# Kernel tuning notes

Measured on AMD Instinct MI355X. Metric: run time of the kernel, lower is better.

Reference implementation:

```python
import jax, jax.numpy as jnp
import numpy as np

B, S = 1, 1863
D_MODEL, H = 1024, 16
HD = D_MODEL // H  # 64
MAX_X, MAX_Y, MAX_Z = 32, 32, 8
BASE = 10000.0
MAX_DXY, MAX_DZ = 30, 8
N_PAIRS = HD // 2
PX = N_PAIRS // 3  # 10
PY = N_PAIRS // 3  # 10
PZ = N_PAIRS - PX - PY  # 12


def _rotate_half(x):
    # (x0,x1,x2,x3,...) -> (-x1,x0,-x3,x2,...)
    x1 = x[..., ::2]
    x2 = x[..., 1::2]
    return jnp.stack((-x2, x1), axis=-1).reshape(x.shape)


def _rope_tables(max_pos, dim):
    inv = 1.0 / (BASE ** (np.arange(0, dim, 2, dtype=np.float32) / dim))
    f = np.outer(np.arange(max_pos, dtype=np.float32), inv)
    return jnp.asarray(np.cos(f)), jnp.asarray(np.sin(f))


def setup_inputs() -> dict:
    key = jax.random.key(0)
    ks = jax.random.split(key, 8)
    x = jax.random.normal(ks[0], (B, S, D_MODEL), dtype=jnp.float32)
    Wqkv = jax.random.normal(ks[1], (3 * D_MODEL, D_MODEL), dtype=jnp.float32) * 0.02
    Wout = jax.random.normal(ks[2], (D_MODEL, D_MODEL), dtype=jnp.float32) * 0.02
    bias_x = jax.random.normal(ks[3], (2 * MAX_DXY + 1, H), dtype=jnp.float32) * 0.02
    bias_y = jax.random.normal(ks[4], (2 * MAX_DXY + 1, H), dtype=jnp.float32) * 0.02
    bias_z = jax.random.normal(ks[5], (2 * MAX_DZ + 1, H), dtype=jnp.float32) * 0.02
    pos_xyz = jax.random.randint(ks[6], (B, S, 3), 0, 32, dtype=jnp.int32)
    return {"x": x, "Wqkv": Wqkv, "Wout": Wout, "bias_x": bias_x,
            "bias_y": bias_y, "bias_z": bias_z, "pos_xyz": pos_xyz}


def _apply_rope3d(q, k, pos_xyz):
    cx, sx = _rope_tables(MAX_X, 2 * PX)
    cy, sy = _rope_tables(MAX_Y, 2 * PY)
    cz, sz = _rope_tables(MAX_Z, 2 * PZ)
    xp = jnp.clip(pos_xyz[..., 0], 0, MAX_X - 1)
    yp = jnp.clip(pos_xyz[..., 1], 0, MAX_Y - 1)
    zp = jnp.clip(pos_xyz[..., 2], 0, MAX_Z - 1)
    # [B,S,head_dim] after repeat-interleave(2) per axis, then concat
    cos = jnp.concatenate([jnp.repeat(cx[xp], 2, axis=-1),
                           jnp.repeat(cy[yp], 2, axis=-1),
                           jnp.repeat(cz[zp], 2, axis=-1)], axis=-1)[:, :, None, :]
    sin = jnp.concatenate([jnp.repeat(sx[xp], 2, axis=-1),
                           jnp.repeat(sy[yp], 2, axis=-1),
                           jnp.repeat(sz[zp], 2, axis=-1)], axis=-1)[:, :, None, :]
    q_rot = q * cos + _rotate_half(q) * sin
    k_rot = k * cos + _rotate_half(k) * sin
    return q_rot, k_rot


def reference(x, Wqkv, Wout, bias_x, bias_y, bias_z, pos_xyz):
    b, s, _ = x.shape
    qkv = x @ Wqkv.T  # [B,S,3*D]
    q, k, v = jnp.split(qkv, 3, axis=-1)
    q = q.reshape(b, s, H, HD)
    k = k.reshape(b, s, H, HD)
    v = v.reshape(b, s, H, HD)
    q, k = _apply_rope3d(q, k, pos_xyz)
    scores = jnp.einsum('bqhd,bkhd->bhqk', q, k) * (HD ** -0.5)
    # 3D relative position bias
    px_, py_, pz_ = pos_xyz[..., 0], pos_xyz[..., 1], pos_xyz[..., 2]
    dx = jnp.clip(px_[:, :, None] - px_[:, None, :], -MAX_DXY, MAX_DXY) + MAX_DXY
    dy = jnp.clip(py_[:, :, None] - py_[:, None, :], -MAX_DXY, MAX_DXY) + MAX_DXY
    dz = jnp.clip(pz_[:, :, None] - pz_[:, None, :], -MAX_DZ, MAX_DZ) + MAX_DZ
    bias = (bias_x[dx] + bias_y[dy] + bias_z[dz]).transpose(0, 3, 1, 2)  # [B,H,S,S]
    scores = scores + bias
    causal = jnp.tril(jnp.ones((s, s), dtype=bool))
    scores = jnp.where(causal, scores, -jnp.inf)
    attn = jax.nn.softmax(scores, axis=-1)
    out = jnp.einsum('bhqk,bkhd->bqhd', attn, v).reshape(b, s, D_MODEL)
    return out @ Wout.T
```

## Files before the change

kernel.cpp:

```cpp
#include <hip/hip_runtime.h>

typedef __bf16 bf16;
typedef __bf16 bf16x2 __attribute__((ext_vector_type(2)));
typedef __bf16 bf16x4 __attribute__((ext_vector_type(4)));
typedef __bf16 bf16x8 __attribute__((ext_vector_type(8)));
typedef float  f32x4  __attribute__((ext_vector_type(4)));

#define S_LEN 1863
#define S_PAD 1920
#define DM 1024
#define NH 16
#define HDIM 64
#define AUGD 160
#define KA_STR 168
#define QKV_STRIDE 3072
#define NQT128 15
#define CHUNK 4
#define MAXC 8
#define NQMULTI 13
#define NCHUNK_HEAD 64

#define MFMA_BF16 __builtin_amdgcn_mfma_f32_16x16x32_bf16

__constant__ int QT_BASE[15] = {0, 1, 2, 4, 6, 9, 12, 16, 20, 25, 30, 36, 42, 49, 56};

__device__ __forceinline__ void dma16(const bf16* g, bf16* l) {
  __builtin_amdgcn_global_load_lds(
      (const __attribute__((address_space(1))) unsigned int*)g,
      (__attribute__((address_space(3))) unsigned int*)l, 16, 0, 0);
}

__global__ void cvt3(const float* __restrict__ a, bf16* __restrict__ oa, int na4,
                     const float* __restrict__ b, bf16* __restrict__ ob, int nb4,
                     const float* __restrict__ c, bf16* __restrict__ oc, int nc4) {
  int j = blockIdx.x * blockDim.x + threadIdx.x;
  const float* s; bf16* d;
  if (j < na4) { s = a; d = oa; }
  else {
    j -= na4;
    if (j < nb4) { s = b; d = ob; }
    else { j -= nb4; if (j >= nc4) return; s = c; d = oc; }
  }
  float4 v = ((const float4*)s)[j];
  bf16x4 o;
  o[0] = (bf16)v.x; o[1] = (bf16)v.y; o[2] = (bf16)v.z; o[3] = (bf16)v.w;
  ((bf16x4*)d)[j] = o;
}

template <typename T>
__global__ __launch_bounds__(256) void gemm_bt(const bf16* __restrict__ A,
                                               const bf16* __restrict__ B,
                                               T* __restrict__ C,
                                               int M, int N, int K) {
  __shared__ bf16 As[128][40];
  __shared__ bf16 Bs[64][40];
  const int t = threadIdx.x;
  const int w = t >> 6, l = t & 63;
  const int quad = l >> 4, l16 = l & 15;
  const int wm = w >> 1, wn = w & 1;
  const int bm = blockIdx.y * 128, bn = blockIdx.x * 64;

  f32x4 acc[4][2];
#pragma unroll
  for (int mi = 0; mi < 4; ++mi)
#pragma unroll
    for (int ni = 0; ni < 2; ++ni) acc[mi][ni] = 0;

  const int srow = t >> 2;
  const int sk8  = (t & 3) * 8;

  for (int k0 = 0; k0 < K; k0 += 32) {
    bf16x8 a0 = *(const bf16x8*)&A[(size_t)min(bm + srow,      M - 1) * K + k0 + sk8];
    bf16x8 a1 = *(const bf16x8*)&A[(size_t)min(bm + srow + 64, M - 1) * K + k0 + sk8];
    bf16x8 b0 = *(const bf16x8*)&B[(size_t)(bn + srow) * K + k0 + sk8];
    __syncthreads();
    *(bf16x8*)&As[srow][sk8]      = a0;
    *(bf16x8*)&As[srow + 64][sk8] = a1;
    *(bf16x8*)&Bs[srow][sk8]      = b0;
    __syncthreads();

    bf16x8 af[4], bfr[2];
#pragma unroll
    for (int mi = 0; mi < 4; ++mi) af[mi]  = *(bf16x8*)&As[wm * 64 + mi * 16 + l16][quad * 8];
#pragma unroll
    for (int ni = 0; ni < 2; ++ni) bfr[ni] = *(bf16x8*)&Bs[wn * 32 + ni * 16 + l16][quad * 8];
#pragma unroll
    for (int mi = 0; mi < 4; ++mi)
#pragma unroll
      for (int ni = 0; ni < 2; ++ni)
        acc[mi][ni] = MFMA_BF16(af[mi], bfr[ni], acc[mi][ni], 0, 0, 0);
  }

#pragma unroll
  for (int mi = 0; mi < 4; ++mi)
#pragma unroll
    for (int r = 0; r < 4; ++r) {
      int m = bm + wm * 64 + mi * 16 + quad * 4 + r;
      if (m < M) {
#pragma unroll
        for (int ni = 0; ni < 2; ++ni)
          C[(size_t)m * N + bn + wn * 32 + ni * 16 + l16] = (T)acc[mi][ni][r];
      }
    }
}

__global__ __launch_bounds__(256) void gemm_bt64(const bf16* __restrict__ A,
                                                 const bf16* __restrict__ B,
                                                 float* __restrict__ C,
                                                 int M, int N, int K) {
  __shared__ bf16 As[64][40];
  __shared__ bf16 Bs[64][40];
  const int t = threadIdx.x;
  const int w = t >> 6, l = t & 63;
  const int quad = l >> 4, l16 = l & 15;
  const int wm = w >> 1, wn = w & 1;
  const int bm = blockIdx.y * 64, bn = blockIdx.x * 64;

  f32x4 acc[2][2];
#pragma unroll
  for (int mi = 0; mi < 2; ++mi)
#pragma unroll
    for (int ni = 0; ni < 2; ++ni) acc[mi][ni] = 0;

  const int srow = t >> 2;
  const int sk8  = (t & 3) * 8;

  for (int k0 = 0; k0 < K; k0 += 32) {
    bf16x8 a0 = *(const bf16x8*)&A[(size_t)min(bm + srow, M - 1) * K + k0 + sk8];
    bf16x8 b0 = *(const bf16x8*)&B[(size_t)(bn + srow) * K + k0 + sk8];
    __syncthreads();
    *(bf16x8*)&As[srow][sk8] = a0;
    *(bf16x8*)&Bs[srow][sk8] = b0;
    __syncthreads();

    bf16x8 af[2], bfr[2];
#pragma unroll
    for (int mi = 0; mi < 2; ++mi) af[mi]  = *(bf16x8*)&As[wm * 32 + mi * 16 + l16][quad * 8];
#pragma unroll
    for (int ni = 0; ni < 2; ++ni) bfr[ni] = *(bf16x8*)&Bs[wn * 32 + ni * 16 + l16][quad * 8];
#pragma unroll
    for (int mi = 0; mi < 2; ++mi)
#pragma unroll
      for (int ni = 0; ni < 2; ++ni)
        acc[mi][ni] = MFMA_BF16(af[mi], bfr[ni], acc[mi][ni], 0, 0, 0);
  }

#pragma unroll
  for (int mi = 0; mi < 2; ++mi)
#pragma unroll
    for (int r = 0; r < 4; ++r) {
      int m = bm + wm * 32 + mi * 16 + quad * 4 + r;
      if (m < M) {
#pragma unroll
        for (int ni = 0; ni < 2; ++ni)
          C[(size_t)m * N + bn + wn * 32 + ni * 16 + l16] = acc[mi][ni][r];
      }
    }
}

__global__ __launch_bounds__(256) void pack_all(const bf16* __restrict__ qkv,
                                                const int* __restrict__ pos,
                                                const float* __restrict__ bxg,
                                                const float* __restrict__ byg,
                                                const float* __restrict__ bzg,
                                                bf16* __restrict__ Qa,
                                                bf16* __restrict__ Ka,
                                                bf16* __restrict__ Vt) {
  const int st = blockIdx.x, h = blockIdx.y;
  const int t = threadIdx.x;
  __shared__ float bxs[61], bys[61], bzs[17];
  __shared__ float vtile[64][68];

  if (t < 61) { bxs[t] = bxg[t * NH + h]; bys[t] = byg[t * NH + h]; }
  if (t < 17) bzs[t] = bzg[t * NH + h];

  for (int i = t; i < 1024; i += 256) {
    int row = i >> 4, c4 = (i & 15) * 4;
    int sg = min(st * 64 + row, S_LEN - 1);
    bf16x4 v = *(const bf16x4*)&qkv[(size_t)sg * QKV_STRIDE + 2 * DM + h * HDIM + c4];
    *(float4*)&vtile[row][c4] = make_float4((float)v[0], (float)v[1], (float)v[2], (float)v[3]);
  }
  __syncthreads();

  for (int i = t; i < 2048; i += 256) {
    const int sl = i >> 5, sub = i & 31;
    const int s = st * 64 + sl;
    const int sc = min(s, S_LEN - 1);
    const int px = pos[sc * 3 + 0], py = pos[sc * 3 + 1], pz = pos[sc * 3 + 2];
    int j, P, pp;
    if (sub < 10)      { j = sub;      P = 10; pp = min(max(px, 0), 31); }
    else if (sub < 20) { j = sub - 10; P = 10; pp = min(max(py, 0), 31); }
    else               { j = sub - 20; P = 12; pp = min(max(pz, 0), 7);  }
    const float inv = __expf(-(float)j / (float)P * 9.210340371976184f);
    const float ang = (float)pp * inv;
    float sn, cs;
    __sincosf(ang, &sn, &cs);
    const size_t base = (size_t)sc * QKV_STRIDE + h * HDIM + 2 * sub;
    bf16x2 q2 = *(const bf16x2*)&qkv[base];
    bf16x2 k2 = *(const bf16x2*)&qkv[base + DM];
    float q0 = (float)q2[0], q1 = (float)q2[1];
    float k0 = (float)k2[0], k1 = (float)k2[1];
    const size_t qb = ((size_t)h * S_PAD + s) * AUGD;
    const size_t kb = ((size_t)h * S_PAD + s) * KA_STR;
    bf16x2 oq, ok;
    oq[0] = (bf16)((q0 * cs - q1 * sn) * 0.125f);
    oq[1] = (bf16)((q1 * cs + q0 * sn) * 0.125f);
    ok[0] = (bf16)(k0 * cs - k1 * sn);
    ok[1] = (bf16)(k1 * cs + k0 * sn);
    *(bf16x2*)&Qa[qb + 2 * sub] = oq;
    *(bf16x2*)&Ka[kb + 2 * sub] = ok;

    const int ix = min(max(px - sub, -30), 30) + 30;
    const int iy = min(max(py - sub, -30), 30) + 30;
    const int iz = min(max(pz - sub, -8), 8) + 8;
    Qa[qb + 64 + sub]  = (bf16)bxs[ix];
    Qa[qb + 96 + sub]  = (bf16)bys[iy];
    Qa[qb + 128 + sub] = (bf16)bzs[iz];
    Ka[kb + 64 + sub]  = (bf16)(sub == px ? 1.0f : 0.0f);
    Ka[kb + 96 + sub]  = (bf16)(sub == py ? 1.0f : 0.0f);
    Ka[kb + 128 + sub] = (bf16)(sub == pz ? 1.0f : 0.0f);
  }

  for (int i = t; i < 1024; i += 256) {
    int d = i >> 4, s4 = (i & 15) * 4;
    bf16x4 o;
    o[0] = (bf16)vtile[s4 + 0][d];
    o[1] = (bf16)vtile[s4 + 1][d];
    o[2] = (bf16)vtile[s4 + 2][d];
    o[3] = (bf16)vtile[s4 + 3][d];
    *(bf16x4*)&Vt[((size_t)h * HDIM + d) * S_PAD + st * 64 + s4] = o;
  }
}

__global__ __launch_bounds__(256) void attn_split(const bf16* __restrict__ Qa,
                                                  const bf16* __restrict__ Ka,
                                                  const bf16* __restrict__ Vt,
                                                  bf16* __restrict__ outb,
                                                  float* __restrict__ Opart,
                                                  float* __restrict__ lpart) {
  const int b = blockIdx.x;
  const int h = b & 15;
  const int id = 63 - (b >> 4);
  int qt = 14;
  while (QT_BASE[qt] > id) --qt;
  const int c = id - QT_BASE[qt];
  const int chain = 2 * qt + 2;
  const int k0 = c * CHUNK;
  const int kend = min(k0 + CHUNK, chain);

  const int t = threadIdx.x, w = t >> 6, l = t & 63;
  const int quad = l >> 4, l16 = l & 15;

  __shared__ bf16 Ks[64][KA_STR];
  __shared__ bf16 Vs[64][72];
  __shared__ bf16 Ps[4][16][72];

  bf16x8 aq[2][5];
  int ig[2][4];
#pragma unroll
  for (int mi = 0; mi < 2; ++mi) {
    const int qrow = qt * 128 + w * 32 + mi * 16 + l16;
    const bf16* qp = &Qa[((size_t)h * S_PAD + qrow) * AUGD + quad * 8];
#pragma unroll
    for (int sg = 0; sg < 5; ++sg) aq[mi][sg] = *(const bf16x8*)(qp + sg * 32);
#pragma unroll
    for (int r = 0; r < 4; ++r) ig[mi][r] = qt * 128 + w * 32 + mi * 16 + quad * 4 + r;
  }

  f32x4 O[2][4];
#pragma unroll
  for (int mi = 0; mi < 2; ++mi)
#pragma unroll
    for (int di = 0; di < 4; ++di) O[mi][di] = 0;
  float lacc[2][4] = {};

  bf16* KsF = &Ks[0][0];

  for (int kt = k0; kt < kend; ++kt) {
    __syncthreads();
    {
      const bf16* gtile = &Ka[((size_t)h * S_PAD + kt * 64) * KA_STR];
#pragma unroll
      for (int seg = 0; seg < 6; ++seg) {
        int sidx = w + seg * 4;
        if (sidx < 21) dma16(gtile + sidx * 512 + l * 8, KsF + sidx * 512);
      }
    }
    for (int i = t; i < 512; i += 256) {
      int row = i >> 3, c8 = (i & 7) * 8;
      *(bf16x8*)&Vs[row][c8] =
          *(const bf16x8*)&Vt[((size_t)h * HDIM + row) * S_PAD + kt * 64 + c8];
    }
    __syncthreads();

    f32x4 sf[2][4];
#pragma unroll
    for (int ni = 0; ni < 4; ++ni) {
      bf16x8 bk[5];
      const bf16* kp = &Ks[ni * 16 + l16][quad * 8];
#pragma unroll
      for (int sg = 0; sg < 5; ++sg) bk[sg] = *(const bf16x8*)(kp + sg * 32);
#pragma unroll
      for (int mi = 0; mi < 2; ++mi) {
        f32x4 z = {0.f, 0.f, 0.f, 0.f};
#pragma unroll
        for (int sg = 0; sg < 5; ++sg) z = MFMA_BF16(aq[mi][sg], bk[sg], z, 0, 0, 0);
        sf[mi][ni] = z;
      }
    }

#pragma unroll
    for (int mi = 0; mi < 2; ++mi) {
      const bool msk = (kt * 64 + 63) > (qt * 128 + w * 32 + mi * 16);
#pragma unroll
      for (int ni = 0; ni < 4; ++ni) {
        const int jg = kt * 64 + ni * 16 + l16;
#pragma unroll
        for (int r = 0; r < 4; ++r) {
          float p = __expf(sf[mi][ni][r]);
          if (msk && jg > ig[mi][r]) p = 0.f;
          lacc[mi][r] += p;
          Ps[w][quad * 4 + r][ni * 16 + l16] = (bf16)p;
        }
      }
      bf16x8 ap0 = *(bf16x8*)&Ps[w][l16][quad * 8];
      bf16x8 ap1 = *(bf16x8*)&Ps[w][l16][32 + quad * 8];
#pragma unroll
      for (int di = 0; di < 4; ++di) {
        bf16x8 bv0 = *(bf16x8*)&Vs[di * 16 + l16][quad * 8];
        bf16x8 bv1 = *(bf16x8*)&Vs[di * 16 + l16][32 + quad * 8];
        O[mi][di] = MFMA_BF16(ap0, bv0, O[mi][di], 0, 0, 0);
        O[mi][di] = MFMA_BF16(ap1, bv1, O[mi][di], 0, 0, 0);
      }
    }
  }

#pragma unroll
  for (int mi = 0; mi < 2; ++mi)
#pragma unroll
    for (int r = 0; r < 4; ++r) {
      float v = lacc[mi][r];
      v += __shfl_xor(v, 1);
      v += __shfl_xor(v, 2);
      v += __shfl_xor(v, 4);
      v += __shfl_xor(v, 8);
      lacc[mi][r] = v;
    }

  if (k0 == 0 && kend == chain) {
#pragma unroll
    for (int mi = 0; mi < 2; ++mi)
#pragma unroll
      for (int r = 0; r < 4; ++r) {
        const int row = ig[mi][r];
        if (row < S_LEN) {
          const float inv = 1.0f / lacc[mi][r];
#pragma unroll
          for (int di = 0; di < 4; ++di)
            outb[(size_t)row * DM + h * HDIM + di * 16 + l16] = (bf16)(O[mi][di][r] * inv);
        }
      }
  } else {
    float* ob = Opart + (((size_t)h * NQMULTI + (qt - 2)) * MAXC + c) * 8192;
#pragma unroll
    for (int mi = 0; mi < 2; ++mi)
#pragma unroll
      for (int r = 0; r < 4; ++r) {
        const int row32 = w * 32 + mi * 16 + quad * 4 + r;
#pragma unroll
        for (int di = 0; di < 4; ++di)
          ob[row32 * 64 + di * 16 + l16] = O[mi][di][r];
      }
    if (l16 == 0) {
      float* lb = lpart + (((size_t)h * NQMULTI + (qt - 2)) * MAXC + c) * 128;
#pragma unroll
      for (int mi = 0; mi < 2; ++mi)
#pragma unroll
        for (int r = 0; r < 4; ++r) lb[w * 32 + mi * 16 + quad * 4 + r] = lacc[mi][r];
    }
  }
}

__global__ __launch_bounds__(256) void attn_combine(const float* __restrict__ Opart,
                                                    const float* __restrict__ lpart,
                                                    bf16* __restrict__ outb) {
  const int qt = blockIdx.x + 2;
  const int h = blockIdx.y;
  const int t = threadIdx.x;
  const int row = t >> 1, half = t & 1;
  const int nchunk = (2 * qt + 5) >> 2;
  float4 acc[8];
#pragma unroll
  for (int j = 0; j < 8; ++j) acc[j] = make_float4(0.f, 0.f, 0.f, 0.f);
  float lsum = 0.f;
  const size_t pb = ((size_t)h * NQMULTI + (qt - 2)) * MAXC;
  for (int cc = 0; cc < nchunk; ++cc) {
    const float4* p4 = (const float4*)(Opart + (pb + cc) * 8192 + row * 64 + half * 32);
#pragma unroll
    for (int j = 0; j < 8; ++j) {
      float4 v = p4[j];
      acc[j].x += v.x; acc[j].y += v.y; acc[j].z += v.z; acc[j].w += v.w;
    }
    lsum += lpart[(pb + cc) * 128 + row];
  }
  const int s = qt * 128 + row;
  if (s < S_LEN) {
    const float inv = 1.0f / lsum;
    bf16* op = outb + (size_t)s * DM + h * HDIM + half * 32;
#pragma unroll
    for (int j = 0; j < 8; ++j) {
      bf16x4 o;
      o[0] = (bf16)(acc[j].x * inv);
      o[1] = (bf16)(acc[j].y * inv);
      o[2] = (bf16)(acc[j].z * inv);
      o[3] = (bf16)(acc[j].w * inv);
      *(bf16x4*)&op[j * 4] = o;
    }
  }
}

extern "C" void kernel_launch(void* const* d_in, const int* in_sizes, int n_in,
                              void* d_out, int out_size, void* d_ws, size_t ws_size,
                              hipStream_t stream) {
  const float* x    = (const float*)d_in[0];
  const float* Wqkv = (const float*)d_in[1];
  const float* Wout = (const float*)d_in[2];
  const float* bx   = (const float*)d_in[3];
  const float* by   = (const float*)d_in[4];
  const float* bz   = (const float*)d_in[5];
  const int*   pos  = (const int*)d_in[6];
  float* out = (float*)d_out;

  char* ws = (char*)d_ws;
  float* Opart = (float*)ws;
  bf16* xb    = (bf16*)ws;
  bf16* wqkvb = xb + (size_t)S_LEN * DM;
  bf16* qkvb  = wqkvb + (size_t)QKV_STRIDE * DM;
  ws += (size_t)NH * NQMULTI * MAXC * 8192 * 4;
  bf16* woutb = (bf16*)ws;   ws += (size_t)DM * DM * 2;
  bf16* Qaug  = (bf16*)ws;   ws += (size_t)NH * S_PAD * AUGD * 2;
  bf16* Kaug  = (bf16*)ws;   ws += (size_t)NH * S_PAD * KA_STR * 2;
  bf16* Vtb   = (bf16*)ws;   ws += (size_t)NH * S_PAD * HDIM * 2;
  bf16* attnb = (bf16*)ws;   ws += (size_t)S_LEN * DM * 2;
  float* lpart = (float*)ws; ws += (size_t)NH * NQMULTI * MAXC * 128 * 4;

  const int na4 = S_LEN * DM / 4, nb4 = QKV_STRIDE * DM / 4, nc4 = DM * DM / 4;
  const int ntot = na4 + nb4 + nc4;
  cvt3<<<dim3((ntot + 255) / 256), 256, 0, stream>>>(x, xb, na4, Wqkv, wqkvb, nb4, Wout, woutb, nc4);
  gemm_bt<bf16><<<dim3(QKV_STRIDE / 64, NQT128), 256, 0, stream>>>(
      xb, wqkvb, qkvb, S_LEN, QKV_STRIDE, DM);
  pack_all<<<dim3(S_PAD / 64, NH), 256, 0, stream>>>(qkvb, pos, bx, by, bz, Qaug, Kaug, Vtb);
  attn_split<<<dim3(NH * NCHUNK_HEAD), 256, 0, stream>>>(Qaug, Kaug, Vtb, attnb, Opart, lpart);
  attn_combine<<<dim3(NQMULTI, NH), 256, 0, stream>>>(Opart, lpart, attnb);
  gemm_bt64<<<dim3(DM / 64, (S_LEN + 63) / 64), 256, 0, stream>>>(
      attnb, woutb, out, S_LEN, DM, DM);
}
```

Before: 174.3 us.

## Keep attention P in registers via transposed scores; DMA GEMM tiles; bf16 partials

The attention kernel now computes transposed score tiles (keys by queries), so the exponentiated probabilities already sit in the register layout of the B operand of a 16x16x16 bf16 MFMA. This removes the LDS round trip through the Ps buffer and shrinks the row-sum reduction to two shuffles. Split-chunk partial outputs are written and read as bf16 instead of fp32, halving combine traffic at some precision cost. Both GEMMs stage tiles with global_load_lds DMA into unpadded LDS arrays instead of register loads and stores, which may add LDS bank conflicts on the fragment reads.

```diff
diff --git a/kernel.cpp b/kernel.cpp
--- a/kernel.cpp
+++ b/kernel.cpp
@@ -5,6 +5,7 @@
 typedef __bf16 bf16x4 __attribute__((ext_vector_type(4)));
 typedef __bf16 bf16x8 __attribute__((ext_vector_type(8)));
 typedef float  f32x4  __attribute__((ext_vector_type(4)));
+typedef short  short4v __attribute__((ext_vector_type(4)));
 
 #define S_LEN 1863
 #define S_PAD 1920
@@ -21,6 +22,7 @@
 #define NCHUNK_HEAD 64
 
 #define MFMA_BF16 __builtin_amdgcn_mfma_f32_16x16x32_bf16
+#define MFMA_BF16_K16 __builtin_amdgcn_mfma_f32_16x16x16bf16_1k
 
 __constant__ int QT_BASE[15] = {0, 1, 2, 4, 6, 9, 12, 16, 20, 25, 30, 36, 42, 49, 56};
 
@@ -28,6 +30,10 @@
   __builtin_amdgcn_global_load_lds(
       (const __attribute__((address_space(1))) unsigned int*)g,
       (__attribute__((address_space(3))) unsigned int*)l, 16, 0, 0);
+}
+
+__device__ __forceinline__ short4v as_s4(bf16x4 v) {
+  return __builtin_bit_cast(short4v, v);
 }
 
 __global__ void cvt3(const float* __restrict__ a, bf16* __restrict__ oa, int na4,
@@ -52,13 +58,15 @@
                                                const bf16* __restrict__ B,
                                                T* __restrict__ C,
                                                int M, int N, int K) {
-  __shared__ bf16 As[128][40];
-  __shared__ bf16 Bs[64][40];
+  __shared__ bf16 As[128][32];
+  __shared__ bf16 Bs[64][32];
   const int t = threadIdx.x;
   const int w = t >> 6, l = t & 63;
   const int quad = l >> 4, l16 = l & 15;
   const int wm = w >> 1, wn = w & 1;
   const int bm = blockIdx.y * 128, bn = blockIdx.x * 64;
+  const int lr = l >> 2;
+  const int lc = (l & 3) * 8;
 
   f32x4 acc[4][2];
 #pragma unroll
@@ -66,17 +74,15 @@
 #pragma unroll
     for (int ni = 0; ni < 2; ++ni) acc[mi][ni] = 0;
 
-  const int srow = t >> 2;
-  const int sk8  = (t & 3) * 8;
-
   for (int k0 = 0; k0 < K; k0 += 32) {
-    bf16x8 a0 = *(const bf16x8*)&A[(size_t)min(bm + srow,      M - 1) * K + k0 + sk8];
-    bf16x8 a1 = *(const bf16x8*)&A[(size_t)min(bm + srow + 64, M - 1) * K + k0 + sk8];
-    bf16x8 b0 = *(const bf16x8*)&B[(size_t)(bn + srow) * K + k0 + sk8];
-    __syncthreads();
-    *(bf16x8*)&As[srow][sk8]      = a0;
-    *(bf16x8*)&As[srow + 64][sk8] = a1;
-    *(bf16x8*)&Bs[srow][sk8]      = b0;
+    __syncthreads();
+#pragma unroll
+    for (int p = 0; p < 2; ++p) {
+      const int seg = 2 * w + p;
+      const int row = seg * 16 + lr;
+      dma16(&A[(size_t)min(bm + row, M - 1) * K + k0 + lc], &As[seg * 16][0]);
+    }
+    dma16(&B[(size_t)(bn + w * 16 + lr) * K + k0 + lc], &Bs[w * 16][0]);
     __syncthreads();
 
     bf16x8 af[4], bfr[2];
@@ -108,13 +114,15 @@
                                                  const bf16* __restrict__ B,
                                                  float* __restrict__ C,
                                                  int M, int N, int K) {
-  __shared__ bf16 As[64][40];
-  __shared__ bf16 Bs[64][40];
+  __shared__ bf16 As[64][32];
+  __shared__ bf16 Bs[64][32];
   const int t = threadIdx.x;
   const int w = t >> 6, l = t & 63;
   const int quad = l >> 4, l16 = l & 15;
   const int wm = w >> 1, wn = w & 1;
   const int bm = blockIdx.y * 64, bn = blockIdx.x * 64;
+  const int lr = l >> 2;
+  const int lc = (l & 3) * 8;
 
   f32x4 acc[2][2];
 #pragma unroll
@@ -122,15 +130,10 @@
 #pragma unroll
     for (int ni = 0; ni < 2; ++ni) acc[mi][ni] = 0;
 
-  const int srow = t >> 2;
-  const int sk8  = (t & 3) * 8;
-
   for (int k0 = 0; k0 < K; k0 += 32) {
-    bf16x8 a0 = *(const bf16x8*)&A[(size_t)min(bm + srow, M - 1) * K + k0 + sk8];
-    bf16x8 b0 = *(const bf16x8*)&B[(size_t)(bn + srow) * K + k0 + sk8];
-    __syncthreads();
-    *(bf16x8*)&As[srow][sk8] = a0;
-    *(bf16x8*)&Bs[srow][sk8] = b0;
+    __syncthreads();
+    dma16(&A[(size_t)min(bm + w * 16 + lr, M - 1) * K + k0 + lc], &As[w * 16][0]);
+    dma16(&B[(size_t)(bn + w * 16 + lr) * K + k0 + lc], &Bs[w * 16][0]);
     __syncthreads();
 
     bf16x8 af[2], bfr[2];
@@ -236,7 +239,7 @@
                                                   const bf16* __restrict__ Ka,
                                                   const bf16* __restrict__ Vt,
                                                   bf16* __restrict__ outb,
-                                                  float* __restrict__ Opart,
+                                                  bf16* __restrict__ Opart,
                                                   float* __restrict__ lpart) {
   const int b = blockIdx.x;
   const int h = b & 15;
@@ -253,18 +256,16 @@
 
   __shared__ bf16 Ks[64][KA_STR];
   __shared__ bf16 Vs[64][72];
-  __shared__ bf16 Ps[4][16][72];
-
-  bf16x8 aq[2][5];
-  int ig[2][4];
+
+  bf16x8 bq[2][5];
+  int igm[2];
 #pragma unroll
   for (int mi = 0; mi < 2; ++mi) {
     const int qrow = qt * 128 + w * 32 + mi * 16 + l16;
+    igm[mi] = qrow;
     const bf16* qp = &Qa[((size_t)h * S_PAD + qrow) * AUGD + quad * 8];
 #pragma unroll
-    for (int sg = 0; sg < 5; ++sg) aq[mi][sg] = *(const bf16x8*)(qp + sg * 32);
-#pragma unroll
-    for (int r = 0; r < 4; ++r) ig[mi][r] = qt * 128 + w * 32 + mi * 16 + quad * 4 + r;
+    for (int sg = 0; sg < 5; ++sg) bq[mi][sg] = *(const bf16x8*)(qp + sg * 32);
   }
 
   f32x4 O[2][4];
@@ -272,7 +273,7 @@
   for (int mi = 0; mi < 2; ++mi)
 #pragma unroll
     for (int di = 0; di < 4; ++di) O[mi][di] = 0;
-  float lacc[2][4] = {};
+  float lacc[2] = {0.f, 0.f};
 
   bf16* KsF = &Ks[0][0];
 
@@ -296,92 +297,92 @@
     f32x4 sf[2][4];
 #pragma unroll
     for (int ni = 0; ni < 4; ++ni) {
-      bf16x8 bk[5];
+      bf16x8 ak[5];
       const bf16* kp = &Ks[ni * 16 + l16][quad * 8];
 #pragma unroll
-      for (int sg = 0; sg < 5; ++sg) bk[sg] = *(const bf16x8*)(kp + sg * 32);
+      for (int sg = 0; sg < 5; ++sg) ak[sg] = *(const bf16x8*)(kp + sg * 32);
 #pragma unroll
       for (int mi = 0; mi < 2; ++mi) {
         f32x4 z = {0.f, 0.f, 0.f, 0.f};
 #pragma unroll
-        for (int sg = 0; sg < 5; ++sg) z = MFMA_BF16(aq[mi][sg], bk[sg], z, 0, 0, 0);
+        for (int sg = 0; sg < 5; ++sg) z = MFMA_BF16(ak[sg], bq[mi][sg], z, 0, 0, 0);
         sf[mi][ni] = z;
       }
     }
 
+    short4v pf[2][4];
+#pragma unroll
+    for (int mi = 0; mi < 2; ++mi)
+#pragma unroll
+      for (int ni = 0; ni < 4; ++ni) {
+        bf16x4 pb;
+#pragma unroll
+        for (int r = 0; r < 4; ++r) {
+          const int key = kt * 64 + ni * 16 + quad * 4 + r;
+          float p = __expf(sf[mi][ni][r]);
+          if (key > igm[mi]) p = 0.f;
+          lacc[mi] += p;
+          pb[r] = (bf16)p;
+        }
+        pf[mi][ni] = as_s4(pb);
+      }
+
+#pragma unroll
+    for (int g = 0; g < 4; ++g)
+#pragma unroll
+      for (int di = 0; di < 4; ++di) {
+        short4v vf = as_s4(*(const bf16x4*)&Vs[di * 16 + l16][g * 16 + quad * 4]);
+#pragma unroll
+        for (int mi = 0; mi < 2; ++mi)
+          O[mi][di] = MFMA_BF16_K16(vf, pf[mi][g], O[mi][di], 0, 0, 0);
+      }
+  }
+
+#pragma unroll
+  for (int mi = 0; mi < 2; ++mi) {
+    float v = lacc[mi];
+    v += __shfl_xor(v, 16);
+    v += __shfl_xor(v, 32);
+    lacc[mi] = v;
+  }
+
+  if (k0 == 0 && kend == chain) {
 #pragma unroll
     for (int mi = 0; mi < 2; ++mi) {
-      const bool msk = (kt * 64 + 63) > (qt * 128 + w * 32 + mi * 16);
-#pragma unroll
-      for (int ni = 0; ni < 4; ++ni) {
-        const int jg = kt * 64 + ni * 16 + l16;
-#pragma unroll
-        for (int r = 0; r < 4; ++r) {
-          float p = __expf(sf[mi][ni][r]);
-          if (msk && jg > ig[mi][r]) p = 0.f;
-          lacc[mi][r] += p;
-          Ps[w][quad * 4 + r][ni * 16 + l16] = (bf16)p;
+      const int qrow = igm[mi];
+      if (qrow < S_LEN) {
+        const float inv = 1.0f / lacc[mi];
+#pragma unroll
+        for (int di = 0; di < 4; ++di) {
+          bf16x4 o;
+#pragma unroll
+          for (int r = 0; r < 4; ++r) o[r] = (bf16)(O[mi][di][r] * inv);
+          *(bf16x4*)&outb[(size_t)qrow * DM + h * HDIM + di * 16 + quad * 4] = o;
         }
       }
-      bf16x8 ap0 = *(bf16x8*)&Ps[w][l16][quad * 8];
-      bf16x8 ap1 = *(bf16x8*)&Ps[w][l16][32 + quad * 8];
+    }
+  } else {
+    bf16* ob = Opart + (((size_t)h * NQMULTI + (qt - 2)) * MAXC + c) * 8192;
+#pragma unroll
+    for (int mi = 0; mi < 2; ++mi) {
+      const int row32 = w * 32 + mi * 16 + l16;
 #pragma unroll
       for (int di = 0; di < 4; ++di) {
-        bf16x8 bv0 = *(bf16x8*)&Vs[di * 16 + l16][quad * 8];
-        bf16x8 bv1 = *(bf16x8*)&Vs[di * 16 + l16][32 + quad * 8];
-        O[mi][di] = MFMA_BF16(ap0, bv0, O[mi][di], 0, 0, 0);
-        O[mi][di] = MFMA_BF16(ap1, bv1, O[mi][di], 0, 0, 0);
-      }
-    }
-  }
-
-#pragma unroll
-  for (int mi = 0; mi < 2; ++mi)
-#pragma unroll
-    for (int r = 0; r < 4; ++r) {
-      float v = lacc[mi][r];
-      v += __shfl_xor(v, 1);
-      v += __shfl_xor(v, 2);
-      v += __shfl_xor(v, 4);
-      v += __shfl_xor(v, 8);
-      lacc[mi][r] = v;
-    }
-
-  if (k0 == 0 && kend == chain) {
-#pragma unroll
-    for (int mi = 0; mi < 2; ++mi)
-#pragma unroll
-      for (int r = 0; r < 4; ++r) {
-        const int row = ig[mi][r];
-        if (row < S_LEN) {
-          const float inv = 1.0f / lacc[mi][r];
-#pragma unroll
-          for (int di = 0; di < 4; ++di)
-            outb[(size_t)row * DM + h * HDIM + di * 16 + l16] = (bf16)(O[mi][di][r] * inv);
-        }
-      }
-  } else {
-    float* ob = Opart + (((size_t)h * NQMULTI + (qt - 2)) * MAXC + c) * 8192;
-#pragma unroll
-    for (int mi = 0; mi < 2; ++mi)
-#pragma unroll
-      for (int r = 0; r < 4; ++r) {
-        const int row32 = w * 32 + mi * 16 + quad * 4 + r;
-#pragma unroll
-        for (int di = 0; di < 4; ++di)
-          ob[row32 * 64 + di * 16 + l16] = O[mi][di][r];
-      }
-    if (l16 == 0) {
+        bf16x4 o;
+#pragma unroll
+        for (int r = 0; r < 4; ++r) o[r] = (bf16)O[mi][di][r];
+        *(bf16x4*)&ob[row32 * 64 + di * 16 + quad * 4] = o;
+      }
+    }
+    if (quad == 0) {
       float* lb = lpart + (((size_t)h * NQMULTI + (qt - 2)) * MAXC + c) * 128;
 #pragma unroll
-      for (int mi = 0; mi < 2; ++mi)
-#pragma unroll
-        for (int r = 0; r < 4; ++r) lb[w * 32 + mi * 16 + quad * 4 + r] = lacc[mi][r];
-    }
-  }
-}
-
-__global__ __launch_bounds__(256) void attn_combine(const float* __restrict__ Opart,
+      for (int mi = 0; mi < 2; ++mi) lb[w * 32 + mi * 16 + l16] = lacc[mi];
+    }
+  }
+}
+
+__global__ __launch_bounds__(256) void attn_combine(const bf16* __restrict__ Opart,
                                                     const float* __restrict__ lpart,
                                                     bf16* __restrict__ outb) {
   const int qt = blockIdx.x + 2;
@@ -389,17 +390,18 @@
   const int t = threadIdx.x;
   const int row = t >> 1, half = t & 1;
   const int nchunk = (2 * qt + 5) >> 2;
-  float4 acc[8];
-#pragma unroll
-  for (int j = 0; j < 8; ++j) acc[j] = make_float4(0.f, 0.f, 0.f, 0.f);
+  float acc[32];
+#pragma unroll
+  for (int j = 0; j < 32; ++j) acc[j] = 0.f;
   float lsum = 0.f;
   const size_t pb = ((size_t)h * NQMULTI + (qt - 2)) * MAXC;
   for (int cc = 0; cc < nchunk; ++cc) {
-    const float4* p4 = (const float4*)(Opart + (pb + cc) * 8192 + row * 64 + half * 32);
-#pragma unroll
-    for (int j = 0; j < 8; ++j) {
-      float4 v = p4[j];
-      acc[j].x += v.x; acc[j].y += v.y; acc[j].z += v.z; acc[j].w += v.w;
+    const bf16x8* p8 = (const bf16x8*)(Opart + (pb + cc) * 8192 + row * 64 + half * 32);
+#pragma unroll
+    for (int j = 0; j < 4; ++j) {
+      bf16x8 v = p8[j];
+#pragma unroll
+      for (int e = 0; e < 8; ++e) acc[j * 8 + e] += (float)v[e];
     }
     lsum += lpart[(pb + cc) * 128 + row];
   }
@@ -410,10 +412,10 @@
 #pragma unroll
     for (int j = 0; j < 8; ++j) {
       bf16x4 o;
-      o[0] = (bf16)(acc[j].x * inv);
-      o[1] = (bf16)(acc[j].y * inv);
-      o[2] = (bf16)(acc[j].z * inv);
-      o[3] = (bf16)(acc[j].w * inv);
+      o[0] = (bf16)(acc[j * 4 + 0] * inv);
+      o[1] = (bf16)(acc[j * 4 + 1] * inv);
+      o[2] = (bf16)(acc[j * 4 + 2] * inv);
+      o[3] = (bf16)(acc[j * 4 + 3] * inv);
       *(bf16x4*)&op[j * 4] = o;
     }
   }
@@ -432,11 +434,11 @@
   float* out = (float*)d_out;
 
   char* ws = (char*)d_ws;
-  float* Opart = (float*)ws;
+  bf16* Opart = (bf16*)ws;
   bf16* xb    = (bf16*)ws;
   bf16* wqkvb = xb + (size_t)S_LEN * DM;
   bf16* qkvb  = wqkvb + (size_t)QKV_STRIDE * DM;
-  ws += (size_t)NH * NQMULTI * MAXC * 8192 * 4;
+  ws += (size_t)NH * NQMULTI * MAXC * 8192 * 2;
   bf16* woutb = (bf16*)ws;   ws += (size_t)DM * DM * 2;
   bf16* Qaug  = (bf16*)ws;   ws += (size_t)NH * S_PAD * AUGD * 2;
   bf16* Kaug  = (bf16*)ws;   ws += (size_t)NH * S_PAD * KA_STR * 2;
```

New measurement: 166.7 us. 4.4% less time.
